# Optimization experiments

Measured on AMD Instinct MI355X. Metric: run time of the kernel, lower is better.

## Reference

```python
import jax, jax.numpy as jnp
import numpy as np
from jax import lax

C = 128      # channels
H = 128
W = 128
B = 2
WS = 4       # window size
HEADS = 4
HID = int(C * 2.66)  # 340
EPS = 1e-6


def conv1x1(x, w):
    # x: [b,c,h,w], w: [out,in]
    return jnp.einsum('oc,bchw->bohw', w, x)


def dwconv3(x, w):
    # depthwise 3x3, w: [c,1,3,3]
    return lax.conv_general_dilated(
        x, w, window_strides=(1, 1), padding='SAME',
        feature_group_count=x.shape[1],
        dimension_numbers=('NCHW', 'OIHW', 'NCHW'))


def layernorm(x, w, b):
    # channel-wise LN over dim 1 (per pixel), w/b: [C]
    m = x.mean(axis=1, keepdims=True)
    v = ((x - m) ** 2).mean(axis=1, keepdims=True)
    xn = (x - m) / jnp.sqrt(v + EPS)
    return xn * w[None, :, None, None] + b[None, :, None, None]


def l2norm(x):
    n = jnp.sqrt(jnp.sum(x * x, axis=-1, keepdims=True))
    return x / jnp.maximum(n, 1e-12)


def rsa(x, qkv_w, dw_w, proj_w, temp):
    b, c, h, w = x.shape
    ws = WS
    x_ = jnp.roll(x, (-ws // 2, -ws // 2), axis=(2, 3))  # shifts > 0
    qkv = dwconv3(conv1x1(x_, qkv_w), dw_w)
    q, k, v = jnp.split(qkv, 3, axis=1)

    def win(t):  # b c (h dh) (w dw) -> b (h w) (dh dw) c
        return t.reshape(b, c, h // ws, ws, w // ws, ws) \
                .transpose(0, 2, 4, 3, 5, 1) \
                .reshape(b, (h // ws) * (w // ws), ws * ws, c)

    q, k, v = win(q), win(k), win(v)
    q = l2norm(q)
    k = l2norm(k)
    # attn = q^T @ k  -> [b, nw, c, c]
    attn = jax.nn.relu(jnp.einsum('bnpc,bnpd->bncd', q, k) * temp[0, 0, 0])
    out = jnp.einsum('bnpc,bncd->bnpd', v, attn)  # v @ attn
    out = out.reshape(b, h // ws, w // ws, ws, ws, c) \
             .transpose(0, 5, 1, 3, 2, 4).reshape(b, c, h, w)
    out = jnp.roll(out, (ws // 2, ws // 2), axis=(2, 3))
    return conv1x1(out, proj_w)


def gsa(x, qkv_w, dw_w, proj_w, temp):
    b, c, h, w = x.shape
    hd = HEADS
    ch = c // hd
    qkv = dwconv3(conv1x1(x, qkv_w), dw_w)
    q, k, v = jnp.split(qkv, 3, axis=1)

    def hs(t):  # b (head c) h w -> b head c (h w)
        return t.reshape(b, hd, ch, h * w)

    q, k, v = hs(q), hs(k), hs(v)
    q = l2norm(q)
    k = l2norm(k)
    attn = jax.nn.relu(jnp.einsum('bhcn,bhdn->bhcd', q, k) * temp[0, 0, 0])
    out = jnp.einsum('bhcd,bhdn->bhcn', attn, v).reshape(b, c, h, w)
    return conv1x1(out, proj_w)


def ffn(x, w_in, w_dw, w_out):
    h = dwconv3(conv1x1(x, w_in), w_dw)
    h = jax.nn.gelu(h, approximate=False)
    return conv1x1(h, w_out)


def setup_inputs() -> dict:
    key = jax.random.key(0)
    ks = jax.random.split(key, 16)
    s = 0.05
    d = {
        'x': jax.random.normal(ks[0], (B, C, H, W), jnp.float32),
        # spatial (RSA) branch
        'w_s0': jnp.ones((C,), jnp.float32), 'b_s0': jnp.zeros((C,), jnp.float32),
        'w_s2': jnp.ones((C,), jnp.float32), 'b_s2': jnp.zeros((C,), jnp.float32),
        'rsa_qkv': jax.random.normal(ks[1], (3 * C, C), jnp.float32) * s,
        'rsa_dw': jax.random.normal(ks[2], (3 * C, 1, 3, 3), jnp.float32) * s,
        'rsa_proj': jax.random.normal(ks[3], (C, C), jnp.float32) * s,
        'rsa_temp': jnp.ones((1, 1, 1), jnp.float32),
        'ffs_in': jax.random.normal(ks[4], (HID, C), jnp.float32) * s,
        'ffs_dw': jax.random.normal(ks[5], (HID, 1, 3, 3), jnp.float32) * s,
        'ffs_out': jax.random.normal(ks[6], (C, HID), jnp.float32) * s,
        # channel (GSA) branch
        'w_c0': jnp.ones((C,), jnp.float32), 'b_c0': jnp.zeros((C,), jnp.float32),
        'w_c2': jnp.ones((C,), jnp.float32), 'b_c2': jnp.zeros((C,), jnp.float32),
        'gsa_qkv': jax.random.normal(ks[7], (3 * C, C), jnp.float32) * s,
        'gsa_dw': jax.random.normal(ks[8], (3 * C, 1, 3, 3), jnp.float32) * s,
        'gsa_proj': jax.random.normal(ks[9], (C, C), jnp.float32) * s,
        'gsa_temp': jnp.ones((1, 1, 1), jnp.float32),
        'ffc_in': jax.random.normal(ks[10], (HID, C), jnp.float32) * s,
        'ffc_dw': jax.random.normal(ks[11], (HID, 1, 3, 3), jnp.float32) * s,
        'ffc_out': jax.random.normal(ks[12], (C, HID), jnp.float32) * s,
    }
    return d


def reference(x, w_s0, b_s0, w_s2, b_s2, rsa_qkv, rsa_dw, rsa_proj, rsa_temp,
              ffs_in, ffs_dw, ffs_out,
              w_c0, b_c0, w_c2, b_c2, gsa_qkv, gsa_dw, gsa_proj, gsa_temp,
              ffc_in, ffc_dw, ffc_out):
    # shared_depth = 1: only the i==0 branches execute
    # spatial block (RSA)
    x_ = rsa(layernorm(x, w_s0, b_s0), rsa_qkv, rsa_dw, rsa_proj, rsa_temp)
    x = ffn(layernorm(x_ + x, w_s2, b_s2), ffs_in, ffs_dw, ffs_out) + x_
    # channel block (GSA)
    x_ = gsa(layernorm(x, w_c0, b_c0), gsa_qkv, gsa_dw, gsa_proj, gsa_temp)
    x = ffn(layernorm(x_ + x, w_c2, b_c2), ffc_in, ffc_dw, ffc_out) + x_
    return x
```

## Files before the change

kernel.cpp:

```cpp
#include <hip/hip_runtime.h>
#include <hip/hip_bf16.h>
#include <math.h>

typedef __hip_bfloat16 bf16;
typedef __attribute__((ext_vector_type(8))) short short8;
typedef __attribute__((ext_vector_type(4))) short short4v;
typedef __attribute__((ext_vector_type(4))) float float4v;

static constexpr int cB  = 2;
static constexpr int cC  = 128;
static constexpr int cH  = 128;
static constexpr int cW  = 128;
static constexpr int cP  = cH * cW;
static constexpr int cC3 = 384;
static constexpr int cHID = 340;
static constexpr int cNW = 1024;
static constexpr float cEPS = 1e-6f;

__device__ __forceinline__ float bfu2f(unsigned short u){
  union { unsigned int i; float f; } c; c.i = ((unsigned int)u) << 16; return c.f;
}
__device__ __forceinline__ unsigned short f2b(float f){
  union { float f; unsigned int u; } c; c.f = f;
  unsigned int r = c.u + 0x7FFFu + ((c.u >> 16) & 1u);
  return (unsigned short)(r >> 16);
}

__global__ void k_wcvt(const float* __restrict__ qkv_s, const float* __restrict__ qkv_c,
                       const float* __restrict__ fin_s, const float* __restrict__ fin_c,
                       const float* __restrict__ prj_s, const float* __restrict__ prj_c,
                       const float* __restrict__ fo_s,  const float* __restrict__ fo_c,
                       unsigned short* __restrict__ WB, float* __restrict__ S){
  int i = blockIdx.x * 256 + threadIdx.x;
  if (i >= 319488){
    int j = i - 319488;
    if (j < 8704) S[j] = 0.f;
    return;
  }
  float v;
  if (i < 98304){
    v = (i < 49152) ? qkv_s[i] : qkv_c[i - 49152];
  } else if (i < 196608){
    int j = (i < 147456) ? (i - 98304) : (i - 147456);
    int row = j >> 7, col = j & 127;
    const float* src = (i < 147456) ? fin_s : fin_c;
    v = (row < cHID) ? src[row * 128 + col] : 0.f;
  } else if (i < 229376){
    v = (i < 212992) ? prj_s[i - 196608] : prj_c[i - 212992];
  } else {
    int j = (i < 274432) ? (i - 229376) : (i - 274432);
    int row = j / 352, col = j - row * 352;
    const float* src = (i < 274432) ? fo_s : fo_c;
    v = (col < cHID) ? src[row * cHID + col] : 0.f;
  }
  WB[i] = f2b(v);
}

__global__ void __launch_bounds__(256) k_gemmLN(const unsigned short* __restrict__ Wb,
                                                const float* __restrict__ Xf,
                                                const float* __restrict__ gamma,
                                                const float* __restrict__ beta,
                                                unsigned short* __restrict__ Out){
  __shared__ short Xls[64 * 136];
  __shared__ short Wls[128 * 40];
  __shared__ float gls[128], bls[128];
  __shared__ float psum[64], pssq[64];
  int bid = blockIdx.x;
  int s  = (bid & 7) * 192 + (bid >> 3);
  int mt = s % 3;
  int r3 = s / 3;
  int pt = r3 & 255;
  int b  = r3 >> 8;
  int p0 = pt * 64;
  int m0 = mt * 128;
  int t  = threadIdx.x;
  int px = t & 63, cq = t >> 6;
  if (t < 64){ psum[t] = 0.f; pssq[t] = 0.f; }
  if (t < 128){ gls[t] = gamma[t]; bls[t] = beta[t]; }
  int rh = p0 >> 7, w0 = p0 & 127;
  int hs = (rh + 2) & (cH - 1);
  int sp = hs * cW + ((w0 + 2 + px) & (cW - 1));
  const float* xb = Xf + (size_t)b * cC * cP + sp;
  float xr[32];
  float s1 = 0.f, s2 = 0.f;
  #pragma unroll
  for (int j = 0; j < 32; j++){
    float v = xb[(size_t)(cq * 32 + j) * cP];
    xr[j] = v; s1 += v; s2 += v * v;
  }
  __syncthreads();
  atomicAdd(&psum[px], s1);
  atomicAdd(&pssq[px], s2);
  __syncthreads();
  float mean = psum[px] * (1.f / cC);
  float var  = pssq[px] * (1.f / cC) - mean * mean;
  float rstd = rsqrtf(var + cEPS);
  #pragma unroll
  for (int k = 0; k < 4; k++){
    short8 tv;
    #pragma unroll
    for (int e = 0; e < 8; e++){
      int c = cq * 32 + k * 8 + e;
      tv[e] = (short)f2b((xr[k * 8 + e] - mean) * rstd * gls[c] + bls[c]);
    }
    *(short8*)&Xls[px * 136 + cq * 32 + k * 8] = tv;
  }
  int lanelo = t & 15;
  int quad   = (t >> 4) & 3;
  int wv = t >> 6;
  int w1 = wv & 1;
  int w2 = wv >> 1;
  int srw = t >> 1;
  int kow = (t & 1) * 16;
  float4v acc[2][4];
  #pragma unroll
  for (int i = 0; i < 2; i++)
    #pragma unroll
    for (int j = 0; j < 4; j++)
      acc[i][j] = (float4v){0.f, 0.f, 0.f, 0.f};
  const unsigned short* Wp = Wb + (size_t)(m0 + srw) * 128 + kow;
  short8 a0 = *(const short8*)(Wp);
  short8 a1 = *(const short8*)(Wp + 8);
  for (int k0 = 0; k0 < 128; k0 += 32){
    __syncthreads();
    *(short8*)&Wls[srw * 40 + kow]     = a0;
    *(short8*)&Wls[srw * 40 + kow + 8] = a1;
    __syncthreads();
    if (k0 < 96){
      a0 = *(const short8*)(Wp + k0 + 32);
      a1 = *(const short8*)(Wp + k0 + 40);
    }
    short8 af[2], bfr[4];
    #pragma unroll
    for (int i = 0; i < 2; i++)
      af[i] = *(const short8*)&Xls[(w1 * 32 + i * 16 + lanelo) * 136 + k0 + quad * 8];
    #pragma unroll
    for (int j = 0; j < 4; j++)
      bfr[j] = *(const short8*)&Wls[(w2 * 64 + j * 16 + lanelo) * 40 + quad * 8];
    #pragma unroll
    for (int i = 0; i < 2; i++)
      #pragma unroll
      for (int j = 0; j < 4; j++)
        acc[i][j] = __builtin_amdgcn_mfma_f32_16x16x32_bf16(af[i], bfr[j], acc[i][j], 0, 0, 0);
  }
  __syncthreads();
  #pragma unroll
  for (int i = 0; i < 2; i++)
    #pragma unroll
    for (int j = 0; j < 4; j++){
      int pixloc = w1 * 32 + i * 16 + quad * 4;
      int mloc   = w2 * 64 + j * 16 + lanelo;
      #pragma unroll
      for (int r = 0; r < 4; r++)
        Xls[(pixloc + r) * 136 + mloc] = (short)f2b(acc[i][j][r]);
    }
  __syncthreads();
  unsigned short* Ob = Out + (size_t)b * cP * cC3;
  #pragma unroll
  for (int rr = 0; rr < 4; rr++){
    int id = t + rr * 256;
    int row = id >> 4, col8 = (id & 15) * 8;
    *(short8*)(Ob + (size_t)(p0 + row) * cC3 + m0 + col8) = *(const short8*)&Xls[row * 136 + col8];
  }
}

__global__ void __launch_bounds__(256) k_gemm(const unsigned short* __restrict__ Wb,
                                              const unsigned short* __restrict__ Xg,
                                              unsigned short* __restrict__ Out,
                                              int K, int PK, int PM){
  __shared__ short SMEM[8704];
  short* Wls = SMEM;
  short* Xls = SMEM + 5120;
  int bid = blockIdx.x;
  int s  = (bid & 7) * (1536 >> 3) + (bid >> 3);
  int mt = s % 3;
  int r3 = s / 3;
  int pt = r3 & 255;
  int b  = r3 >> 8;
  int p0 = pt * 64;
  int m0 = mt * 128;
  int t  = threadIdx.x;
  int lanelo = t & 15;
  int quad   = (t >> 4) & 3;
  int wv = t >> 6;
  int w1 = wv & 1;
  int w2 = wv >> 1;
  int srw = t >> 1;
  int kow = (t & 1) * 16;
  int srx = t >> 2;
  int kox = (t & 3) * 8;

  float4v acc[2][4];
  #pragma unroll
  for (int i = 0; i < 2; i++)
    #pragma unroll
    for (int j = 0; j < 4; j++)
      acc[i][j] = (float4v){0.f, 0.f, 0.f, 0.f};

  const unsigned short* Xp = Xg + (size_t)b * cP * PK + (size_t)(p0 + srx) * PK + kox;
  const unsigned short* Wp = Wb + (size_t)(m0 + srw) * K + kow;

  short8 xv  = *(const short8*)(Xp);
  short8 wv0 = *(const short8*)(Wp);
  short8 wv1 = *(const short8*)(Wp + 8);
  for (int k0 = 0; k0 < K; k0 += 32){
    __syncthreads();
    *(short8*)&Wls[srw * 40 + kow]     = wv0;
    *(short8*)&Wls[srw * 40 + kow + 8] = wv1;
    *(short8*)&Xls[srx * 40 + kox]     = xv;
    __syncthreads();
    if (k0 + 32 < K){
      xv  = *(const short8*)(Xp + k0 + 32);
      wv0 = *(const short8*)(Wp + k0 + 32);
      wv1 = *(const short8*)(Wp + k0 + 40);
    }
    short8 af[2], bfr[4];
    #pragma unroll
    for (int i = 0; i < 2; i++)
      af[i] = *(const short8*)&Xls[(w1 * 32 + i * 16 + lanelo) * 40 + quad * 8];
    #pragma unroll
    for (int j = 0; j < 4; j++)
      bfr[j] = *(const short8*)&Wls[(w2 * 64 + j * 16 + lanelo) * 40 + quad * 8];
    #pragma unroll
    for (int i = 0; i < 2; i++)
      #pragma unroll
      for (int j = 0; j < 4; j++)
        acc[i][j] = __builtin_amdgcn_mfma_f32_16x16x32_bf16(af[i], bfr[j], acc[i][j], 0, 0, 0);
  }
  __syncthreads();
  #pragma unroll
  for (int i = 0; i < 2; i++)
    #pragma unroll
    for (int j = 0; j < 4; j++){
      int pixloc = w1 * 32 + i * 16 + quad * 4;
      int mloc   = w2 * 64 + j * 16 + lanelo;
      #pragma unroll
      for (int r = 0; r < 4; r++)
        SMEM[(pixloc + r) * 136 + mloc] = (short)f2b(acc[i][j][r]);
    }
  __syncthreads();
  unsigned short* Ob = Out + (size_t)b * cP * PM;
  #pragma unroll
  for (int rr = 0; rr < 4; rr++){
    int id = t + rr * 256;
    int row = id >> 4, col8 = (id & 15) * 8;
    int wcol = m0 + col8;
    if (wcol < PM)
      *(short8*)(Ob + (size_t)(p0 + row) * PM + wcol) = *(const short8*)&SMEM[row * 136 + col8];
  }
}

template<int MODE>
__global__ void __launch_bounds__(256) k_gemm64(const unsigned short* __restrict__ Wb,
                                                const unsigned short* __restrict__ Xg,
                                                const float* __restrict__ R,
                                                const float* __restrict__ Base,
                                                const float* __restrict__ gamma,
                                                const float* __restrict__ beta,
                                                float* __restrict__ Tr,
                                                unsigned short* __restrict__ LNo,
                                                int K, int PK){
  __shared__ short SMEM[8704];
  __shared__ float gls[128], bls[128];
  __shared__ float psum[64], pssq[64];
  short* Wls = SMEM;
  short* Xls = SMEM + 5120;
  int b  = blockIdx.z;
  int p0 = blockIdx.x * 64;
  int t  = threadIdx.x;
  int lanelo = t & 15;
  int quad   = (t >> 4) & 3;
  int wv = t >> 6;
  int w2 = wv >> 1, w1 = wv & 1;
  int srw = t >> 1;
  int kow = (t & 1) * 16;
  int srx = t >> 2;
  int kox = (t & 3) * 8;

  if (MODE != 3){
    if (t < 128){ gls[t] = gamma[t]; bls[t] = beta[t]; }
    if (t < 64){ psum[t] = 0.f; pssq[t] = 0.f; }
  }

  float4v acc[4][2];
  #pragma unroll
  for (int i = 0; i < 4; i++){
    acc[i][0] = (float4v){0.f, 0.f, 0.f, 0.f};
    acc[i][1] = (float4v){0.f, 0.f, 0.f, 0.f};
  }
  const unsigned short* Xp = Xg + (size_t)b * cP * PK + (size_t)(p0 + srx) * PK + kox;
  const unsigned short* Wp = Wb + (size_t)srw * K + kow;

  short8 xv  = *(const short8*)(Xp);
  short8 wv0 = *(const short8*)(Wp);
  short8 wv1 = *(const short8*)(Wp + 8);
  for (int k0 = 0; k0 < K; k0 += 32){
    __syncthreads();
    *(short8*)&Wls[srw * 40 + kow]     = wv0;
    *(short8*)&Wls[srw * 40 + kow + 8] = wv1;
    *(short8*)&Xls[srx * 40 + kox]     = xv;
    __syncthreads();
    if (k0 + 32 < K){
      xv  = *(const short8*)(Xp + k0 + 32);
      wv0 = *(const short8*)(Wp + k0 + 32);
      wv1 = *(const short8*)(Wp + k0 + 40);
    }
    short8 af[4], bfr[2];
    #pragma unroll
    for (int i = 0; i < 4; i++)
      af[i] = *(const short8*)&Wls[(w2 * 64 + i * 16 + lanelo) * 40 + quad * 8];
    #pragma unroll
    for (int j = 0; j < 2; j++)
      bfr[j] = *(const short8*)&Xls[(w1 * 32 + j * 16 + lanelo) * 40 + quad * 8];
    #pragma unroll
    for (int i = 0; i < 4; i++)
      #pragma unroll
      for (int j = 0; j < 2; j++)
        acc[i][j] = __builtin_amdgcn_mfma_f32_16x16x32_bf16(af[i], bfr[j], acc[i][j], 0, 0, 0);
  }
  float lnv[4][2][4];
  #pragma unroll
  for (int i = 0; i < 4; i++)
    #pragma unroll
    for (int j = 0; j < 2; j++){
      int n = p0 + w1 * 32 + j * 16 + lanelo;
      #pragma unroll
      for (int r = 0; r < 4; r++){
        int m = w2 * 64 + i * 16 + quad * 4 + r;
        size_t idx = (size_t)b * cC * cP + (size_t)m * cP + n;
        float v = acc[i][j][r];
        if (MODE >= 2) v += R[idx];
        Tr[idx] = v;
        if (MODE == 1) v += Base[idx];
        lnv[i][j][r] = v;
      }
    }
  if (MODE == 3) return;
  __syncthreads();
  #pragma unroll
  for (int j = 0; j < 2; j++){
    int nl = w1 * 32 + j * 16 + lanelo;
    float s = 0.f, ss = 0.f;
    #pragma unroll
    for (int i = 0; i < 4; i++)
      #pragma unroll
      for (int r = 0; r < 4; r++){
        float v = lnv[i][j][r];
        s += v; ss += v * v;
      }
    atomicAdd(&psum[nl], s);
    atomicAdd(&pssq[nl], ss);
  }
  __syncthreads();
  #pragma unroll
  for (int j = 0; j < 2; j++){
    int nl = w1 * 32 + j * 16 + lanelo;
    float mean = psum[nl] * (1.f / cC);
    float var = pssq[nl] * (1.f / cC) - mean * mean;
    float rstd = rsqrtf(var + cEPS);
    #pragma unroll
    for (int i = 0; i < 4; i++)
      #pragma unroll
      for (int r = 0; r < 4; r++){
        int m = w2 * 64 + i * 16 + quad * 4 + r;
        SMEM[nl * 136 + m] = (short)f2b((lnv[i][j][r] - mean) * rstd * gls[m] + bls[m]);
      }
  }
  __syncthreads();
  unsigned short* Ob = LNo + (size_t)b * cP * cC;
  #pragma unroll
  for (int rr = 0; rr < 4; rr++){
    int id = t + rr * 256;
    int row = id >> 4, col8 = (id & 15) * 8;
    short8 sv = *(const short8*)&SMEM[row * 136 + col8];
    *(short8*)(Ob + (size_t)(p0 + row) * cC + col8) = sv;
  }
}

template<int GELU, int CCn, int PITCH>
__global__ void __launch_bounds__(256) k_dw(const unsigned short* __restrict__ in,
                                            const float* __restrict__ wt,
                                            unsigned short* __restrict__ out){
  __shared__ float wls[16 * 76];
  int t = threadIdx.x;
  int cbase = blockIdx.y * 128;
  for (int i = t; i < 16 * 72; i += 256){
    int cg = i / 72, rem = i - cg * 72;
    int tap = rem >> 3, j = rem & 7;
    int c = cbase + cg * 8 + j;
    wls[cg * 76 + rem] = (c < CCn) ? wt[c * 9 + tap] : 0.f;
  }
  __syncthreads();
  int cgl = t & 15, pixl = t >> 4;
  int c0 = cbase + cgl * 8;
  if (c0 >= PITCH) return;
  int p = blockIdx.x * 16 + pixl;
  int h = p >> 7, w = p & 127;
  int b = blockIdx.z;
  const unsigned short* ib = in + (size_t)b * cP * PITCH;
  float4 wreg[18];
  #pragma unroll
  for (int q = 0; q < 18; q++)
    wreg[q] = *(const float4*)&wls[cgl * 76 + q * 4];
  short8 v[9];
  #pragma unroll
  for (int ky = 0; ky < 3; ky++){
    int hh = h + ky - 1;
    bool okh = (unsigned)hh < (unsigned)cH;
    int hc = okh ? hh : h;
    #pragma unroll
    for (int kx = 0; kx < 3; kx++){
      int ww = w + kx - 1;
      bool okw = (unsigned)ww < (unsigned)cW;
      int wc = okw ? ww : w;
      short8 lv = *(const short8*)(ib + (size_t)(hc * cW + wc) * PITCH + c0);
      if (!(okh && okw)) lv = (short8){0,0,0,0,0,0,0,0};
      v[ky * 3 + kx] = lv;
    }
  }
  float acc[8] = {0,0,0,0,0,0,0,0};
  #pragma unroll
  for (int tap = 0; tap < 9; tap++){
    float4 w0 = wreg[tap * 2];
    float4 w1 = wreg[tap * 2 + 1];
    float wa[8] = {w0.x, w0.y, w0.z, w0.w, w1.x, w1.y, w1.z, w1.w};
    #pragma unroll
    for (int j = 0; j < 8; j++)
      acc[j] += wa[j] * bfu2f((unsigned short)v[tap][j]);
  }
  short8 ov;
  #pragma unroll
  for (int j = 0; j < 8; j++){
    float vv = acc[j];
    if (GELU) vv = 0.5f * vv * (1.f + erff(vv * 0.70710678118654752f));
    ov[j] = (short)f2b(vv);
  }
  *(short8*)(out + (size_t)b * cP * PITCH + (size_t)p * PITCH + c0) = ov;
}

__global__ void __launch_bounds__(256) k_rsadw(const unsigned short* __restrict__ qkv,
                                               const float* __restrict__ wt,
                                               const float* __restrict__ temp,
                                               unsigned short* __restrict__ out){
  constexpr int QT = 0;
  constexpr int KT = 5120;
  constexpr int VO = 10240;
  constexpr int HA = 12416;
  constexpr int AT = 12416;
  __shared__ short lds[26528];
  __shared__ float nq[16], nk[16];
  int blk = blockIdx.x;
  int b  = blk >> 10;
  int nw = blk & 1023;
  int hb = nw >> 5, wb = nw & 31;
  int t = threadIdx.x;
  #pragma unroll
  for (int j = 0; j < 5; j++)
    *(short8*)&lds[t * 40 + j * 8] = (short8){0,0,0,0,0,0,0,0};
  if (t < 16) nq[t] = 0.f;
  else if (t < 32) nk[t - 16] = 0.f;
  __syncthreads();
  const unsigned short* base = qkv + (size_t)b * cP * cC3;
  #pragma unroll
  for (int r = 0; r < 7; r++){
    int i = t + 256 * r;
    if (i < 1728){
      int pix6 = i / 48;
      int cg = i - pix6 * 48;
      int hy = pix6 / 6, wx = pix6 - hy * 6;
      int hh = hb * 4 + hy - 1;
      int ww = wb * 4 + wx - 1;
      short8 v = (short8){0,0,0,0,0,0,0,0};
      if ((unsigned)hh < (unsigned)cH && (unsigned)ww < (unsigned)cW)
        v = *(const short8*)(base + (size_t)(hh * cW + ww) * cC3 + cg * 8);
      *(short8*)&lds[HA + pix6 * 392 + cg * 8] = v;
    }
  }
  __syncthreads();
  {
    int px = t & 15, grp = t >> 4;
    int py = px >> 2, pw = px & 3;
    #pragma unroll
    for (int g = 0; g < 3; g++){
      int c0 = grp * 24 + g * 8;
      const float4* wq = (const float4*)(wt + (size_t)c0 * 9);
      float wa[72];
      #pragma unroll
      for (int q = 0; q < 18; q++){
        float4 v4 = wq[q];
        wa[q * 4 + 0] = v4.x; wa[q * 4 + 1] = v4.y;
        wa[q * 4 + 2] = v4.z; wa[q * 4 + 3] = v4.w;
      }
      float acc8[8] = {0,0,0,0,0,0,0,0};
      #pragma unroll
      for (int ky = 0; ky < 3; ky++)
        #pragma unroll
        for (int kx = 0; kx < 3; kx++){
          short8 iv = *(const short8*)&lds[HA + ((py + ky) * 6 + pw + kx) * 392 + c0];
          int tap = ky * 3 + kx;
          #pragma unroll
          for (int e = 0; e < 8; e++)
            acc8[e] += wa[e * 9 + tap] * bfu2f((unsigned short)iv[e]);
        }
      if (c0 < 256){
        int isQ = c0 < 128;
        int off = isQ ? (QT + c0 * 40) : (KT + (c0 - 128) * 40);
        float s = 0.f;
        #pragma unroll
        for (int e = 0; e < 8; e++){
          unsigned short us = f2b(acc8[e]);
          float f = bfu2f(us);
          s += f * f;
          lds[off + e * 40 + px] = (short)us;
        }
        atomicAdd(isQ ? &nq[px] : &nk[px], s);
      } else {
        short8 sv;
        #pragma unroll
        for (int e = 0; e < 8; e++) sv[e] = (short)f2b(acc8[e]);
        *(short8*)&lds[VO + px * 136 + (c0 - 256)] = sv;
      }
    }
  }
  __syncthreads();
  float T = temp[0];
  #pragma unroll
  for (int r = 0; r < 8; r++){
    int idx = t + 256 * r;
    int c = idx >> 4, p = idx & 15;
    float sc = (1.f / fmaxf(sqrtf(nq[p]), 1e-12f)) * (1.f / fmaxf(sqrtf(nk[p]), 1e-12f));
    int a = QT + c * 40 + p;
    lds[a] = (short)f2b(bfu2f((unsigned short)lds[a]) * sc);
  }
  __syncthreads();
  int lanelo = t & 15;
  int quad = (t >> 4) & 3;
  int wv = t >> 6;
  float4v oacc[2];
  oacc[0] = (float4v){0.f,0.f,0.f,0.f};
  oacc[1] = (float4v){0.f,0.f,0.f,0.f};
  for (int ch = 0; ch < 2; ch++){
    #pragma unroll
    for (int ct = 0; ct < 4; ct++){
      int c0 = ch * 64 + ct * 16;
      short8 af = *(const short8*)&lds[QT + (c0 + lanelo) * 40 + quad * 8];
      #pragma unroll
      for (int dt = 0; dt < 2; dt++){
        int d0 = wv * 32 + dt * 16;
        short8 bf = *(const short8*)&lds[KT + (d0 + lanelo) * 40 + quad * 8];
        float4v acc = __builtin_amdgcn_mfma_f32_16x16x32_bf16(af, bf,
                        (float4v){0.f,0.f,0.f,0.f}, 0, 0, 0);
        short4v sv;
        #pragma unroll
        for (int r2 = 0; r2 < 4; r2++) sv[r2] = (short)f2b(fmaxf(acc[r2] * T, 0.f));
        *(short4v*)&lds[AT + (d0 + lanelo) * 72 + ct * 16 + quad * 4] = sv;
      }
    }
    __syncthreads();
    #pragma unroll
    for (int dt = 0; dt < 2; dt++){
      int d0 = wv * 32 + dt * 16;
      #pragma unroll
      for (int kk = 0; kk < 2; kk++){
        short8 av8 = *(const short8*)&lds[VO + lanelo * 136 + ch * 64 + kk * 32 + quad * 8];
        short8 bv8 = *(const short8*)&lds[AT + (d0 + lanelo) * 72 + kk * 32 + quad * 8];
        oacc[dt] = __builtin_amdgcn_mfma_f32_16x16x32_bf16(av8, bv8, oacc[dt], 0, 0, 0);
      }
    }
    __syncthreads();
  }
  #pragma unroll
  for (int dt = 0; dt < 2; dt++){
    int d = wv * 32 + dt * 16 + lanelo;
    #pragma unroll
    for (int r2 = 0; r2 < 4; r2++){
      int p = quad * 4 + r2;
      lds[p * 136 + d] = (short)f2b(oacc[dt][r2]);
    }
  }
  __syncthreads();
  {
    int px = t >> 4, cg = (t & 15) * 8;
    int h2 = (hb * 4 + (px >> 2) + 2) & (cH - 1);
    int w2 = (wb * 4 + (px & 3) + 2) & (cW - 1);
    short8 sv = *(const short8*)&lds[px * 136 + cg];
    *(short8*)(out + (size_t)b * cP * cC + (size_t)(h2 * cW + w2) * cC + cg) = sv;
  }
}

__global__ void __launch_bounds__(256) k_gramdw(const unsigned short* __restrict__ Ain,
                                                const float* __restrict__ dww,
                                                float* __restrict__ S,
                                                float* __restrict__ Qn,
                                                float* __restrict__ Kn){
  __shared__ float qs[32][132];
  __shared__ float ks[32][132];
  __shared__ float wdw[576];
  int blk = blockIdx.x;
  int chunk = blk & 127;
  int bh = blk >> 7;
  int b = bh >> 2, hd = bh & 3;
  int t = threadIdx.x;
  for (int i = t; i < 576; i += 256){
    int lc = i / 9, tpq = i - lc * 9;
    int c = (lc < 32) ? (hd * 32 + lc) : (128 + hd * 32 + (lc - 32));
    wdw[i] = dww[c * 9 + tpq];
  }
  __syncthreads();
  int row = t >> 1;
  int half = t & 1;
  int h = chunk, w = row;
  const unsigned short* Ab = Ain + (size_t)b * cP * cC3;
  float qa[16], ka[16];
  #pragma unroll
  for (int e = 0; e < 16; e++){ qa[e] = 0.f; ka[e] = 0.f; }
  #pragma unroll
  for (int ky = 0; ky < 3; ky++){
    int hh = h + ky - 1;
    if ((unsigned)hh >= (unsigned)cH) continue;
    #pragma unroll
    for (int kx = 0; kx < 3; kx++){
      int ww = w + kx - 1;
      if ((unsigned)ww >= (unsigned)cW) continue;
      const unsigned short* pp = Ab + (size_t)(hh * cW + ww) * cC3 + hd * 32 + half * 16;
      short8 q0 = *(const short8*)pp;
      short8 q1 = *(const short8*)(pp + 8);
      short8 k0v = *(const short8*)(pp + 128);
      short8 k1v = *(const short8*)(pp + 136);
      int tpi = ky * 3 + kx;
      #pragma unroll
      for (int e = 0; e < 8; e++){
        qa[e]     += wdw[(half * 16 + e) * 9 + tpi]          * bfu2f((unsigned short)q0[e]);
        qa[8 + e] += wdw[(half * 16 + 8 + e) * 9 + tpi]      * bfu2f((unsigned short)q1[e]);
        ka[e]     += wdw[(32 + half * 16 + e) * 9 + tpi]     * bfu2f((unsigned short)k0v[e]);
        ka[8 + e] += wdw[(32 + half * 16 + 8 + e) * 9 + tpi] * bfu2f((unsigned short)k1v[e]);
      }
    }
  }
  #pragma unroll
  for (int e = 0; e < 16; e++){
    qs[half * 16 + e][row] = bfu2f(f2b(qa[e]));
    ks[half * 16 + e][row] = bfu2f(f2b(ka[e]));
  }
  __syncthreads();
  if (t < 64){
    const float* rowp = (t < 32) ? qs[t] : ks[t - 32];
    float s = 0.f;
    #pragma unroll
    for (int i = 0; i < 128; i += 4){
      float4 v = *(const float4*)(rowp + i);
      s += v.x*v.x + v.y*v.y + v.z*v.z + v.w*v.w;
    }
    if (t < 32) atomicAdd(&Qn[bh * 32 + t], s);
    else        atomicAdd(&Kn[bh * 32 + (t - 32)], s);
  }
  int cc = (t >> 4) * 2;
  int dd = t & 15;
  float a00 = 0.f, a01 = 0.f, a10 = 0.f, a11 = 0.f;
  for (int n = 0; n < 128; n += 4){
    float4 q0 = *(const float4*)&qs[cc][n];
    float4 q1 = *(const float4*)&qs[cc + 1][n];
    float4 k0 = *(const float4*)&ks[dd][n];
    float4 k1 = *(const float4*)&ks[dd + 16][n];
    a00 += q0.x*k0.x + q0.y*k0.y + q0.z*k0.z + q0.w*k0.w;
    a01 += q0.x*k1.x + q0.y*k1.y + q0.z*k1.z + q0.w*k1.w;
    a10 += q1.x*k0.x + q1.y*k0.y + q1.z*k0.z + q1.w*k0.w;
    a11 += q1.x*k1.x + q1.y*k1.y + q1.z*k1.z + q1.w*k1.w;
  }
  float* Sb = S + (size_t)bh * 1024;
  atomicAdd(&Sb[cc * 32 + dd], a00);
  atomicAdd(&Sb[cc * 32 + dd + 16], a01);
  atomicAdd(&Sb[(cc + 1) * 32 + dd], a10);
  atomicAdd(&Sb[(cc + 1) * 32 + dd + 16], a11);
}

__global__ void __launch_bounds__(256) k_applydw(const unsigned short* __restrict__ Ain,
                                                 const float* __restrict__ dww,
                                                 const float* __restrict__ S,
                                                 const float* __restrict__ Qn,
                                                 const float* __restrict__ Kn,
                                                 const float* __restrict__ temp,
                                                 unsigned short* __restrict__ out){
  __shared__ short atb[128 * 40];
  __shared__ short OT[64 * 136];
  __shared__ float wdw[1152];
  int b = blockIdx.y;
  int nbase = blockIdx.x * 64;
  int t = threadIdx.x;
  float T = temp[0];
  for (int i = t; i < 1152; i += 256)
    wdw[i] = dww[2304 + i];
  #pragma unroll
  for (int it = 0; it < 16; it++){
    int i = t + it * 256;
    int c = i >> 5, d = i & 31;
    int hd = c >> 5, cl = c & 31;
    int bh = b * 4 + hd;
    float nqv = fmaxf(sqrtf(Qn[bh * 32 + cl]), 1e-12f);
    float nkv = fmaxf(sqrtf(Kn[bh * 32 + d]), 1e-12f);
    float v = fmaxf(S[(size_t)bh * 1024 + cl * 32 + d] / (nqv * nkv) * T, 0.f);
    atb[c * 40 + d] = (short)f2b(v);
  }
  __syncthreads();
  int lanelo = t & 15, quad = (t >> 4) & 3, wv = t >> 6;
  int pix = nbase + wv * 16 + lanelo;
  int h = pix >> 7, w = pix & 127;
  const unsigned short* Ab = Ain + (size_t)b * cP * cC3;
  #pragma unroll
  for (int hd = 0; hd < 4; hd++){
    float va[8] = {0,0,0,0,0,0,0,0};
    #pragma unroll
    for (int ky = 0; ky < 3; ky++){
      int hh = h + ky - 1;
      if ((unsigned)hh >= (unsigned)cH) continue;
      #pragma unroll
      for (int kx = 0; kx < 3; kx++){
        int ww = w + kx - 1;
        if ((unsigned)ww >= (unsigned)cW) continue;
        short8 iv = *(const short8*)(Ab + (size_t)(hh * cW + ww) * cC3 + 256 + hd * 32 + quad * 8);
        int tpi = ky * 3 + kx;
        #pragma unroll
        for (int e = 0; e < 8; e++)
          va[e] += wdw[(hd * 32 + quad * 8 + e) * 9 + tpi] * bfu2f((unsigned short)iv[e]);
      }
    }
    short8 af;
    #pragma unroll
    for (int e = 0; e < 8; e++) af[e] = (short)f2b(va[e]);
    #pragma unroll
    for (int cth = 0; cth < 2; cth++){
      int c0 = hd * 32 + cth * 16;
      short8 bf = *(const short8*)&atb[(c0 + lanelo) * 40 + quad * 8];
      float4v acc = __builtin_amdgcn_mfma_f32_16x16x32_bf16(af, bf,
                      (float4v){0.f,0.f,0.f,0.f}, 0, 0, 0);
      #pragma unroll
      for (int r = 0; r < 4; r++)
        OT[(wv * 16 + quad * 4 + r) * 136 + c0 + lanelo] = (short)f2b(acc[r]);
    }
  }
  __syncthreads();
  unsigned short* ob = out + (size_t)b * cP * cC;
  #pragma unroll
  for (int rr = 0; rr < 4; rr++){
    int id = t + rr * 256;
    int row = id >> 4, col8 = (id & 15) * 8;
    *(short8*)(ob + (size_t)(nbase + row) * cC + col8) = *(const short8*)&OT[row * 136 + col8];
  }
}

extern "C" void kernel_launch(void* const* d_in, const int* in_sizes, int n_in,
                              void* d_out, int out_size, void* d_ws, size_t ws_size,
                              hipStream_t stream){
  const float* x     = (const float*)d_in[0];
  const float* w_s0  = (const float*)d_in[1];
  const float* b_s0  = (const float*)d_in[2];
  const float* w_s2  = (const float*)d_in[3];
  const float* b_s2  = (const float*)d_in[4];
  const float* rsa_qkv  = (const float*)d_in[5];
  const float* rsa_dw   = (const float*)d_in[6];
  const float* rsa_proj = (const float*)d_in[7];
  const float* rsa_temp = (const float*)d_in[8];
  const float* ffs_in   = (const float*)d_in[9];
  const float* ffs_dw   = (const float*)d_in[10];
  const float* ffs_out  = (const float*)d_in[11];
  const float* w_c0  = (const float*)d_in[12];
  const float* b_c0  = (const float*)d_in[13];
  const float* w_c2  = (const float*)d_in[14];
  const float* b_c2  = (const float*)d_in[15];
  const float* gsa_qkv  = (const float*)d_in[16];
  const float* gsa_dw   = (const float*)d_in[17];
  const float* gsa_proj = (const float*)d_in[18];
  const float* gsa_temp = (const float*)d_in[19];
  const float* ffc_in   = (const float*)d_in[20];
  const float* ffc_dw   = (const float*)d_in[21];
  const float* ffc_out  = (const float*)d_in[22];

  const size_t szC  = (size_t)cB * cC * cP;
  const size_t szC3 = (size_t)cB * cC3 * cP;
  float* XF = (float*)d_ws;
  float* XS = XF + szC;
  unsigned short* LO   = (unsigned short*)(XS + szC);
  unsigned short* Abuf = LO + szC;
  unsigned short* Bbuf = Abuf + szC3;
  float* S  = (float*)(Bbuf + szC3);
  float* Qn = S + 8192;
  float* Kn = Qn + 256;
  float* AT = Kn + 256;
  unsigned short* WB = (unsigned short*)(AT + 1024);
  unsigned short* W_QKV_S = WB;
  unsigned short* W_QKV_C = WB + 49152;
  unsigned short* W_FIN_S = WB + 98304;
  unsigned short* W_FIN_C = WB + 147456;
  unsigned short* W_PRJ_S = WB + 196608;
  unsigned short* W_PRJ_C = WB + 212992;
  unsigned short* W_FO_S  = WB + 229376;
  unsigned short* W_FO_C  = WB + 274432;

  dim3 t256(256);
  dim3 gG1(cP / 64 * 3 * cB);
  dim3 gG64(cP / 64, 1, cB);
  dim3 gDW(cP / 16, 3, cB);

  k_wcvt<<<dim3(1282), t256, 0, stream>>>(rsa_qkv, gsa_qkv, ffs_in, ffc_in,
                                          rsa_proj, gsa_proj, ffs_out, ffc_out, WB, S);

  k_gemmLN<<<gG1, t256, 0, stream>>>(W_QKV_S, x, w_s0, b_s0, Abuf);
  k_rsadw<<<dim3(cB * cNW), t256, 0, stream>>>(Abuf, rsa_dw, rsa_temp, LO);
  k_gemm64<1><<<gG64, t256, 0, stream>>>(W_PRJ_S, LO, nullptr, x, w_s2, b_s2, XS, LO, 128, 128);
  k_gemm<<<gG1, t256, 0, stream>>>(W_FIN_S, LO, Abuf, 128, 128, 352);
  k_dw<1,340,352><<<gDW, t256, 0, stream>>>(Abuf, ffs_dw, Bbuf);
  k_gemm64<2><<<gG64, t256, 0, stream>>>(W_FO_S, Bbuf, XS, nullptr, w_c0, b_c0, XF, LO, 352, 352);

  k_gemm<<<gG1, t256, 0, stream>>>(W_QKV_C, LO, Abuf, 128, 128, 384);
  k_gramdw<<<dim3(1024), t256, 0, stream>>>(Abuf, gsa_dw, S, Qn, Kn);
  k_applydw<<<dim3(cP / 64, cB), t256, 0, stream>>>(Abuf, gsa_dw, S, Qn, Kn, gsa_temp, LO);
  k_gemm64<1><<<gG64, t256, 0, stream>>>(W_PRJ_C, LO, nullptr, XF, w_c2, b_c2, XS, LO, 128, 128);
  k_gemm<<<gG1, t256, 0, stream>>>(W_FIN_C, LO, Abuf, 128, 128, 352);
  k_dw<1,340,352><<<gDW, t256, 0, stream>>>(Abuf, ffc_dw, Bbuf);
  k_gemm64<3><<<gG64, t256, 0, stream>>>(W_FO_C, Bbuf, XS, nullptr, nullptr, nullptr,
                                         (float*)d_out, nullptr, 352, 352);
}
```

Before: 334.2 us.

## Fuse residual+LayerNorm GEMM with following 1x1 conv GEMM in one kernel

Replaces the separate k_gemm64 (projection + residual + LN) and k_gemm (next 1x1 conv) launches with a single k_gfuse kernel. The LN output tile stays in shared memory and feeds the second GEMM directly, so the bf16 LN activation is no longer written to and re-read from global memory. This removes three kernel launches. In exchange, each block uses much more shared memory (about 50KB), which lowers occupancy. The grid for the second GEMM also shrinks to 512 blocks, each looping over three output tiles, where before there were 1536 independent blocks.

Result: faster. 321.6 us, median of 2 (-3.8%).

```diff
diff --git a/kernel.cpp b/kernel.cpp
--- a/kernel.cpp
+++ b/kernel.cpp
@@ -164,89 +164,175 @@
   }
 }
 
-__global__ void __launch_bounds__(256) k_gemm(const unsigned short* __restrict__ Wb,
-                                              const unsigned short* __restrict__ Xg,
-                                              unsigned short* __restrict__ Out,
-                                              int K, int PK, int PM){
-  __shared__ short SMEM[8704];
-  short* Wls = SMEM;
-  short* Xls = SMEM + 5120;
-  int bid = blockIdx.x;
-  int s  = (bid & 7) * (1536 >> 3) + (bid >> 3);
-  int mt = s % 3;
-  int r3 = s / 3;
-  int pt = r3 & 255;
-  int b  = r3 >> 8;
-  int p0 = pt * 64;
-  int m0 = mt * 128;
+template<int MODE>
+__global__ void __launch_bounds__(256) k_gfuse(const unsigned short* __restrict__ W1,
+                                               const unsigned short* __restrict__ Xg,
+                                               const float* __restrict__ R,
+                                               const float* __restrict__ Base,
+                                               const float* __restrict__ gamma,
+                                               const float* __restrict__ beta,
+                                               float* __restrict__ Tr,
+                                               const unsigned short* __restrict__ W2,
+                                               unsigned short* __restrict__ Out2,
+                                               int K1, int PK1, int PITCH2, int M2LIM){
+  __shared__ short SM[25088];
+  __shared__ float gls[128], bls[128];
+  __shared__ float psum[64], pssq[64];
+  short* XA = SM;
+  short* WA = SM + 2560;
+  short* XB = SM + 7680;
+  short* OB = SM + 16384;
+  int b  = blockIdx.z;
+  int p0 = blockIdx.x * 64;
   int t  = threadIdx.x;
   int lanelo = t & 15;
   int quad   = (t >> 4) & 3;
   int wv = t >> 6;
-  int w1 = wv & 1;
-  int w2 = wv >> 1;
+  int w2 = wv >> 1, w1 = wv & 1;
   int srw = t >> 1;
   int kow = (t & 1) * 16;
   int srx = t >> 2;
   int kox = (t & 3) * 8;
 
-  float4v acc[2][4];
-  #pragma unroll
-  for (int i = 0; i < 2; i++)
-    #pragma unroll
-    for (int j = 0; j < 4; j++)
-      acc[i][j] = (float4v){0.f, 0.f, 0.f, 0.f};
-
-  const unsigned short* Xp = Xg + (size_t)b * cP * PK + (size_t)(p0 + srx) * PK + kox;
-  const unsigned short* Wp = Wb + (size_t)(m0 + srw) * K + kow;
-
+  if (t < 128){ gls[t] = gamma[t]; bls[t] = beta[t]; }
+  if (t < 64){ psum[t] = 0.f; pssq[t] = 0.f; }
+
+  float4v acc[4][2];
+  #pragma unroll
+  for (int i = 0; i < 4; i++){
+    acc[i][0] = (float4v){0.f, 0.f, 0.f, 0.f};
+    acc[i][1] = (float4v){0.f, 0.f, 0.f, 0.f};
+  }
+  const unsigned short* Xp = Xg + (size_t)b * cP * PK1 + (size_t)(p0 + srx) * PK1 + kox;
+  const unsigned short* Wp = W1 + (size_t)srw * K1 + kow;
   short8 xv  = *(const short8*)(Xp);
   short8 wv0 = *(const short8*)(Wp);
   short8 wv1 = *(const short8*)(Wp + 8);
-  for (int k0 = 0; k0 < K; k0 += 32){
+  for (int k0 = 0; k0 < K1; k0 += 32){
     __syncthreads();
-    *(short8*)&Wls[srw * 40 + kow]     = wv0;
-    *(short8*)&Wls[srw * 40 + kow + 8] = wv1;
-    *(short8*)&Xls[srx * 40 + kox]     = xv;
+    *(short8*)&WA[srw * 40 + kow]     = wv0;
+    *(short8*)&WA[srw * 40 + kow + 8] = wv1;
+    *(short8*)&XA[srx * 40 + kox]     = xv;
     __syncthreads();
-    if (k0 + 32 < K){
+    if (k0 + 32 < K1){
       xv  = *(const short8*)(Xp + k0 + 32);
       wv0 = *(const short8*)(Wp + k0 + 32);
       wv1 = *(const short8*)(Wp + k0 + 40);
     }
-    short8 af[2], bfr[4];
+    short8 af[4], bfr[2];
+    #pragma unroll
+    for (int i = 0; i < 4; i++)
+      af[i] = *(const short8*)&WA[(w2 * 64 + i * 16 + lanelo) * 40 + quad * 8];
+    #pragma unroll
+    for (int j = 0; j < 2; j++)
+      bfr[j] = *(const short8*)&XA[(w1 * 32 + j * 16 + lanelo) * 40 + quad * 8];
+    #pragma unroll
+    for (int i = 0; i < 4; i++)
+      #pragma unroll
+      for (int j = 0; j < 2; j++)
+        acc[i][j] = __builtin_amdgcn_mfma_f32_16x16x32_bf16(af[i], bfr[j], acc[i][j], 0, 0, 0);
+  }
+  float lnv[4][2][4];
+  #pragma unroll
+  for (int i = 0; i < 4; i++)
+    #pragma unroll
+    for (int j = 0; j < 2; j++){
+      int n = p0 + w1 * 32 + j * 16 + lanelo;
+      #pragma unroll
+      for (int r = 0; r < 4; r++){
+        int m = w2 * 64 + i * 16 + quad * 4 + r;
+        size_t idx = (size_t)b * cC * cP + (size_t)m * cP + n;
+        float v = acc[i][j][r];
+        if (MODE == 2) v += R[idx];
+        Tr[idx] = v;
+        if (MODE == 1) v += Base[idx];
+        lnv[i][j][r] = v;
+      }
+    }
+  __syncthreads();
+  #pragma unroll
+  for (int j = 0; j < 2; j++){
+    int nl = w1 * 32 + j * 16 + lanelo;
+    float s = 0.f, ss = 0.f;
+    #pragma unroll
+    for (int i = 0; i < 4; i++)
+      #pragma unroll
+      for (int r = 0; r < 4; r++){
+        float v = lnv[i][j][r];
+        s += v; ss += v * v;
+      }
+    atomicAdd(&psum[nl], s);
+    atomicAdd(&pssq[nl], ss);
+  }
+  __syncthreads();
+  #pragma unroll
+  for (int j = 0; j < 2; j++){
+    int nl = w1 * 32 + j * 16 + lanelo;
+    float mean = psum[nl] * (1.f / cC);
+    float var = pssq[nl] * (1.f / cC) - mean * mean;
+    float rstd = rsqrtf(var + cEPS);
+    #pragma unroll
+    for (int i = 0; i < 4; i++)
+      #pragma unroll
+      for (int r = 0; r < 4; r++){
+        int m = w2 * 64 + i * 16 + quad * 4 + r;
+        XB[nl * 136 + m] = (short)f2b((lnv[i][j][r] - mean) * rstd * gls[m] + bls[m]);
+      }
+  }
+  const unsigned short* Wq = W2 + (size_t)srw * 128 + kow;
+  short8 b0 = *(const short8*)(Wq);
+  short8 b1 = *(const short8*)(Wq + 8);
+  unsigned short* Ob = Out2 + (size_t)b * cP * PITCH2;
+  for (int mc = 0; mc < 3; mc++){
+    float4v a2[2][4];
     #pragma unroll
     for (int i = 0; i < 2; i++)
-      af[i] = *(const short8*)&Xls[(w1 * 32 + i * 16 + lanelo) * 40 + quad * 8];
-    #pragma unroll
-    for (int j = 0; j < 4; j++)
-      bfr[j] = *(const short8*)&Wls[(w2 * 64 + j * 16 + lanelo) * 40 + quad * 8];
+      #pragma unroll
+      for (int j = 0; j < 4; j++)
+        a2[i][j] = (float4v){0.f, 0.f, 0.f, 0.f};
+    for (int k0 = 0; k0 < 128; k0 += 32){
+      __syncthreads();
+      *(short8*)&WA[srw * 40 + kow]     = b0;
+      *(short8*)&WA[srw * 40 + kow + 8] = b1;
+      __syncthreads();
+      int nk = mc * 128 + k0 + 32;
+      if (nk < 384){
+        const unsigned short* np = W2 + (size_t)((nk >> 7) * 128 + srw) * 128 + (nk & 127) + kow;
+        b0 = *(const short8*)(np);
+        b1 = *(const short8*)(np + 8);
+      }
+      short8 af2[2], bf2[4];
+      #pragma unroll
+      for (int i = 0; i < 2; i++)
+        af2[i] = *(const short8*)&XB[(w1 * 32 + i * 16 + lanelo) * 136 + k0 + quad * 8];
+      #pragma unroll
+      for (int j = 0; j < 4; j++)
+        bf2[j] = *(const short8*)&WA[(w2 * 64 + j * 16 + lanelo) * 40 + quad * 8];
+      #pragma unroll
+      for (int i = 0; i < 2; i++)
+        #pragma unroll
+        for (int j = 0; j < 4; j++)
+          a2[i][j] = __builtin_amdgcn_mfma_f32_16x16x32_bf16(af2[i], bf2[j], a2[i][j], 0, 0, 0);
+    }
     #pragma unroll
     for (int i = 0; i < 2; i++)
       #pragma unroll
-      for (int j = 0; j < 4; j++)
-        acc[i][j] = __builtin_amdgcn_mfma_f32_16x16x32_bf16(af[i], bfr[j], acc[i][j], 0, 0, 0);
-  }
-  __syncthreads();
-  #pragma unroll
-  for (int i = 0; i < 2; i++)
-    #pragma unroll
-    for (int j = 0; j < 4; j++){
-      int pixloc = w1 * 32 + i * 16 + quad * 4;
-      int mloc   = w2 * 64 + j * 16 + lanelo;
-      #pragma unroll
-      for (int r = 0; r < 4; r++)
-        SMEM[(pixloc + r) * 136 + mloc] = (short)f2b(acc[i][j][r]);
-    }
-  __syncthreads();
-  unsigned short* Ob = Out + (size_t)b * cP * PM;
-  #pragma unroll
-  for (int rr = 0; rr < 4; rr++){
-    int id = t + rr * 256;
-    int row = id >> 4, col8 = (id & 15) * 8;
-    int wcol = m0 + col8;
-    if (wcol < PM)
-      *(short8*)(Ob + (size_t)(p0 + row) * PM + wcol) = *(const short8*)&SMEM[row * 136 + col8];
+      for (int j = 0; j < 4; j++){
+        int pixloc = w1 * 32 + i * 16 + quad * 4;
+        int mloc   = w2 * 64 + j * 16 + lanelo;
+        #pragma unroll
+        for (int r = 0; r < 4; r++)
+          OB[(pixloc + r) * 136 + mloc] = (short)f2b(a2[i][j][r]);
+      }
+    __syncthreads();
+    #pragma unroll
+    for (int rr = 0; rr < 4; rr++){
+      int id = t + rr * 256;
+      int row = id >> 4, col8 = (id & 15) * 8;
+      int wcol = mc * 128 + col8;
+      if (wcol < M2LIM)
+        *(short8*)(Ob + (size_t)(p0 + row) * PITCH2 + wcol) = *(const short8*)&OB[row * 136 + col8];
+    }
   }
 }
 
@@ -806,16 +892,16 @@
 
   k_gemmLN<<<gG1, t256, 0, stream>>>(W_QKV_S, x, w_s0, b_s0, Abuf);
   k_rsadw<<<dim3(cB * cNW), t256, 0, stream>>>(Abuf, rsa_dw, rsa_temp, LO);
-  k_gemm64<1><<<gG64, t256, 0, stream>>>(W_PRJ_S, LO, nullptr, x, w_s2, b_s2, XS, LO, 128, 128);
-  k_gemm<<<gG1, t256, 0, stream>>>(W_FIN_S, LO, Abuf, 128, 128, 352);
+  k_gfuse<1><<<gG64, t256, 0, stream>>>(W_PRJ_S, LO, nullptr, x, w_s2, b_s2, XS,
+                                        W_FIN_S, Abuf, 128, 128, 352, 352);
   k_dw<1,340,352><<<gDW, t256, 0, stream>>>(Abuf, ffs_dw, Bbuf);
-  k_gemm64<2><<<gG64, t256, 0, stream>>>(W_FO_S, Bbuf, XS, nullptr, w_c0, b_c0, XF, LO, 352, 352);
-
-  k_gemm<<<gG1, t256, 0, stream>>>(W_QKV_C, LO, Abuf, 128, 128, 384);
+  k_gfuse<2><<<gG64, t256, 0, stream>>>(W_FO_S, Bbuf, XS, nullptr, w_c0, b_c0, XF,
+                                        W_QKV_C, Abuf, 352, 352, 384, 384);
+
   k_gramdw<<<dim3(1024), t256, 0, stream>>>(Abuf, gsa_dw, S, Qn, Kn);
   k_applydw<<<dim3(cP / 64, cB), t256, 0, stream>>>(Abuf, gsa_dw, S, Qn, Kn, gsa_temp, LO);
-  k_gemm64<1><<<gG64, t256, 0, stream>>>(W_PRJ_C, LO, nullptr, XF, w_c2, b_c2, XS, LO, 128, 128);
-  k_gemm<<<gG1, t256, 0, stream>>>(W_FIN_C, LO, Abuf, 128, 128, 352);
+  k_gfuse<1><<<gG64, t256, 0, stream>>>(W_PRJ_C, LO, nullptr, XF, w_c2, b_c2, XS,
+                                        W_FIN_C, Abuf, 128, 128, 352, 352);
   k_dw<1,340,352><<<gDW, t256, 0, stream>>>(Abuf, ffc_dw, Bbuf);
   k_gemm64<3><<<gG64, t256, 0, stream>>>(W_FO_C, Bbuf, XS, nullptr, nullptr, nullptr,
                                          (float*)d_out, nullptr, 352, 352);
```
